# Performance work log

Hardware: AMD Instinct MI355X
Metric: run time of the kernel (lower is better)

Reference implementation:

```python
import jax, jax.numpy as jnp
import numpy as np

NEG_INF = -1.0e9
LN_EPS = 1e-5
LEAK = 0.2


def setup_inputs() -> dict:
    key = jax.random.key(0)
    ks = jax.random.split(key, 8)
    B, C, T, N, H = 8, 64, 24, 512, 2
    hd = C // H
    x = jax.random.normal(ks[0], (B, C, T, N), dtype=jnp.float32)
    gso = jax.random.randint(ks[1], (N, N), 0, 2, dtype=jnp.int32)
    # torch nn.Linear weights are (out, in); xavier-ish scale
    s = (2.0 / (C + C)) ** 0.5
    Wq = jax.random.normal(ks[2], (C, C), dtype=jnp.float32) * s
    Wk = jax.random.normal(ks[3], (C, C), dtype=jnp.float32) * s
    Wv = jax.random.normal(ks[4], (C, C), dtype=jnp.float32) * s
    sa = (2.0 / (H + hd)) ** 0.5
    a_src = jax.random.normal(ks[5], (H, hd), dtype=jnp.float32) * sa
    a_dst = jax.random.normal(ks[6], (H, hd), dtype=jnp.float32) * sa
    ln_gamma = jnp.ones((C,), dtype=jnp.float32)
    ln_beta = jnp.zeros((C,), dtype=jnp.float32)
    return {"x": x, "gso": gso, "Wq": Wq, "Wk": Wk, "Wv": Wv,
            "a_src": a_src, "a_dst": a_dst, "ln_gamma": ln_gamma, "ln_beta": ln_beta}


def _spatial_gat(x, gso, Wq, Wk, Wv, a_src, a_dst, ln_gamma, ln_beta):
    B, C, T, N = x.shape
    H, hd = a_src.shape
    # (B, C, T, N) -> (B*T, N, C)
    xr = jnp.transpose(x, (0, 2, 3, 1)).reshape(B * T, N, C)
    # torch Linear: y = x @ W.T
    Q = jnp.einsum('bnc,dc->bnd', xr, Wq).reshape(B * T, N, H, hd)
    K = jnp.einsum('bnc,dc->bnd', xr, Wk).reshape(B * T, N, H, hd)
    V = jnp.einsum('bnc,dc->bnd', xr, Wv).reshape(B * T, N, H, hd)
    # additive GAT scores, all heads at once
    s_src = jnp.einsum('bnhd,hd->bnh', Q, a_src)  # (BT, N, H)
    s_dst = jnp.einsum('bnhd,hd->bnh', K, a_dst)  # (BT, N, H)
    scores = jax.nn.leaky_relu(s_src[:, :, None, :] + s_dst[:, None, :, :], LEAK)  # (BT, Ni, Nj, H)
    mask = jnp.where(gso == 0, jnp.float32(NEG_INF), jnp.float32(0.0))  # (N, N)
    scores = scores + mask[None, :, :, None]
    attn = jax.nn.softmax(scores, axis=2)  # softmax over destination j
    out = jnp.einsum('bijh,bjhd->bihd', attn, V)  # (BT, N, H, hd)
    out = out.reshape(B * T, N, C)
    # LayerNorm over channel dim
    mu = jnp.mean(out, axis=-1, keepdims=True)
    var = jnp.var(out, axis=-1, keepdims=True)
    out = (out - mu) * jax.lax.rsqrt(var + LN_EPS) * ln_gamma + ln_beta
    # back to (B, C, T, N)
    return jnp.transpose(out.reshape(B, T, N, C), (0, 3, 1, 2))


def reference(x, gso, Wq, Wk, Wv, a_src, a_dst, ln_gamma, ln_beta):
    return _spatial_gat(x, gso, Wq, Wk, Wv, a_src, a_dst, ln_gamma, ln_beta)
```

## Files before the change

### kernel.cpp

```cpp
#include <hip/hip_runtime.h>

#define CDIM 64
#define TDIM 24
#define NDIM 512
#define NBT  192

typedef float    float4v __attribute__((ext_vector_type(4)));
typedef _Float16 half8v  __attribute__((ext_vector_type(8)));
typedef _Float16 half4v  __attribute__((ext_vector_type(4)));
typedef _Float16 half2v  __attribute__((ext_vector_type(2)));


__device__ __forceinline__ float exp2_fast(float x) {
#if __has_builtin(__builtin_amdgcn_exp2f)
  return __builtin_amdgcn_exp2f(x);
#else
  return __expf(x * 0.69314718f);
#endif
}

struct SmemK1 {
  union {
    _Float16 xt[128][72];
    _Float16 vtb[64][136];
  } big;
  _Float16 wv[64][72];
  _Float16 wext[16][72];
};

__launch_bounds__(256, 4)
__global__ void k1_v(const float* __restrict__ x,  const float* __restrict__ Wv,
                     const float* __restrict__ Wq, const float* __restrict__ Wk,
                     const float* __restrict__ a_src, const float* __restrict__ a_dst,
                     const int* __restrict__ gso,
                     _Float16* __restrict__ VT_g,
                     float* __restrict__ s_src_g, float* __restrict__ s_dst_g,
                     unsigned char* __restrict__ maskb) {
  const int t  = threadIdx.x;
  const int bx = blockIdx.x;

  if (bx >= 768) {
    int g = (bx - 768) * 256 + t;
    const int4* gp = (const int4*)gso + (size_t)g * 4;
    unsigned w[4];
#pragma unroll
    for (int k = 0; k < 4; ++k) {
      int4 v = gp[k];
      w[k] = (v.x ? 0x000000FFu : 0u) | (v.y ? 0x0000FF00u : 0u) |
             (v.z ? 0x00FF0000u : 0u) | (v.w ? 0xFF000000u : 0u);
    }
    uint4 o; o.x = w[0]; o.y = w[1]; o.z = w[2]; o.w = w[3];
    ((uint4*)maskb)[g] = o;
    return;
  }

  __shared__ SmemK1 sm;
  const int qn = bx & 3;
  const int bt = bx >> 2;
  const int b  = bt / TDIM, tt = bt % TDIM;
  const int n0 = qn * 128;

#pragma unroll
  for (int it = 0; it < 4; ++it) {
    int idx = it * 256 + t;
    float4 vv = ((const float4*)Wv)[idx];
    int d = idx >> 4, k4 = (idx & 15) * 4;
    half4v h4; h4[0] = (_Float16)vv.x; h4[1] = (_Float16)vv.y;
    h4[2] = (_Float16)vv.z; h4[3] = (_Float16)vv.w;
    *(half4v*)&sm.wv[d][k4] = h4;
  }
  for (int z = t; z < 12 * 72; z += 256) ((_Float16*)sm.wext[4])[z] = (_Float16)0.f;
  if (t < 64) {
    int c = t;
    float s0 = 0.f, s1 = 0.f, d0 = 0.f, d1 = 0.f;
#pragma unroll
    for (int d = 0; d < 32; ++d) {
      s0 += a_src[d]      * Wq[d * 64 + c];
      s1 += a_src[32 + d] * Wq[(32 + d) * 64 + c];
      d0 += a_dst[d]      * Wk[d * 64 + c];
      d1 += a_dst[32 + d] * Wk[(32 + d) * 64 + c];
    }
    const float l2e = 1.44269504f;
    sm.wext[0][c] = (_Float16)(s0 * l2e); sm.wext[1][c] = (_Float16)(s1 * l2e);
    sm.wext[2][c] = (_Float16)(d0 * l2e); sm.wext[3][c] = (_Float16)(d1 * l2e);
  }
  for (int it = 0; it < 16; ++it) {
    int idx = it * 256 + t;
    int cp = idx >> 7, n = idx & 127;
    int c0 = cp * 2;
    const float* base = x + ((size_t)(b * CDIM + c0) * TDIM + tt) * NDIM + n0 + n;
    half2v p; p[0] = (_Float16)base[0]; p[1] = (_Float16)base[(size_t)TDIM * NDIM];
    *(half2v*)&sm.big.xt[n][c0] = p;
  }
  __syncthreads();

  const int lane = t & 63, w = t >> 6;
  const int m = lane & 15, quad = lane >> 4;
  const int mbase = w * 32;

  float4v acc[2][5];
#pragma unroll
  for (int mt = 0; mt < 2; ++mt)
#pragma unroll
    for (int nt = 0; nt < 5; ++nt)
#pragma unroll
      for (int r = 0; r < 4; ++r) acc[mt][nt][r] = 0.f;

#pragma unroll
  for (int ks = 0; ks < 2; ++ks) {
    half8v af[2], bf[5];
#pragma unroll
    for (int mt = 0; mt < 2; ++mt)
      af[mt] = *(const half8v*)&sm.big.xt[mbase + mt * 16 + m][ks * 32 + quad * 8];
#pragma unroll
    for (int nt = 0; nt < 4; ++nt)
      bf[nt] = *(const half8v*)&sm.wv[nt * 16 + m][ks * 32 + quad * 8];
    bf[4] = *(const half8v*)&sm.wext[m][ks * 32 + quad * 8];
#pragma unroll
    for (int mt = 0; mt < 2; ++mt)
#pragma unroll
      for (int nt = 0; nt < 5; ++nt)
        acc[mt][nt] = __builtin_amdgcn_mfma_f32_16x16x32_f16(af[mt], bf[nt], acc[mt][nt], 0, 0, 0);
  }

  if (m < 4) {
    float* basep = (m < 2 ? s_src_g : s_dst_g) + (size_t)(bt * 2 + (m & 1)) * NDIM;
#pragma unroll
    for (int mt = 0; mt < 2; ++mt)
#pragma unroll
      for (int r = 0; r < 4; ++r)
        basep[n0 + mbase + mt * 16 + quad * 4 + r] = acc[mt][4][r];
  }
  __syncthreads();

#pragma unroll
  for (int mt = 0; mt < 2; ++mt)
#pragma unroll
    for (int nt = 0; nt < 4; ++nt)
#pragma unroll
      for (int r = 0; r < 4; r += 2) {
        int nl = mbase + mt * 16 + quad * 4 + r;
        int c  = nt * 16 + m;
        half2v p = __builtin_bit_cast(half2v,
            __builtin_amdgcn_cvt_pkrtz(acc[mt][nt][r], acc[mt][nt][r + 1]));
        *(half2v*)&sm.big.vtb[c][nl] = p;
      }
  __syncthreads();

  const uint4* vq = (const uint4*)sm.big.vtb;
#pragma unroll
  for (int it = 0; it < 4; ++it) {
    int idx = it * 256 + t;
    int c = idx >> 4, q4 = idx & 15;
    ((uint4*)VT_g)[(size_t)(bt * 64 + c) * 64 + qn * 16 + q4] = vq[c * 17 + q4];
  }
}

struct SmemK2 {
  union {
    struct { _Float16 vt[64][128]; } s;
    struct { float otile[128][66]; float rsum[2][128]; float rsq[2][128];
             float mu[128]; float rs[128]; } e;
  } u;
  _Float16 sF16[2][512];
  _Float16 sP16[2][512];
};

__launch_bounds__(256, 3)
__global__ void k2_attn(const _Float16* __restrict__ VT_g,
                        const float* __restrict__ s_src_g, const float* __restrict__ s_dst_g,
                        const unsigned char* __restrict__ maskb,
                        const float* __restrict__ gamma, const float* __restrict__ beta,
                        float* __restrict__ out) {
  __shared__ SmemK2 sm;
  const int t     = threadIdx.x;
  const int id    = blockIdx.x;
  const int itile = (id >> 3) & 3;
  const int bt    = ((id >> 5) << 3) | (id & 7);
  const int i0    = itile * 128;
  const int b     = bt / TDIM, tt = bt % TDIM;
  const int lane  = t & 63, w = t >> 6;
  const int h = w >> 1, ihalf = w & 1;
  const int m = lane & 15, quad = lane >> 4;
  const int rbase = ihalf * 64;

  for (int it = 0; it < 4; ++it) {
    int idx = it * 256 + t;
    float d = s_dst_g[(size_t)bt * 2 * NDIM + idx];
    ((_Float16*)sm.sF16)[idx] = (_Float16)exp2_fast(d);
    ((_Float16*)sm.sP16)[idx] = (_Float16)exp2_fast(0.2f * d);
  }
  half2v e2[4], q2[4];
#pragma unroll
  for (int mt = 0; mt < 4; ++mt) {
    float sv = s_src_g[(size_t)(bt * 2 + h) * NDIM + i0 + rbase + mt * 16 + m];
    _Float16 ev = (_Float16)exp2_fast(sv - 6.f);
    _Float16 qv = (_Float16)exp2_fast(0.2f * sv - 6.f);
    e2[mt][0] = ev; e2[mt][1] = ev;
    q2[mt][0] = qv; q2[mt][1] = qv;
  }

  float4v acc[4][2], accs[4];
#pragma unroll
  for (int mt = 0; mt < 4; ++mt)
#pragma unroll
    for (int r = 0; r < 4; ++r) { acc[mt][0][r] = 0.f; acc[mt][1][r] = 0.f; accs[mt][r] = 0.f; }
  const half8v bones = {(_Float16)1.f, (_Float16)1.f, (_Float16)1.f, (_Float16)1.f,
                        (_Float16)1.f, (_Float16)1.f, (_Float16)1.f, (_Float16)1.f};

  const uint4* vsrc = (const uint4*)VT_g;
  uint4 pv0, pv1, pv2, pv3;
  const int vc  = t >> 4;
  const int vch = t & 15;
  const int vswz = (vch * 8) ^ ((vc & 7) * 8);

  const unsigned char* mrow = maskb + (size_t)(i0 + rbase + m) * NDIM + quad * 8;
  uint2 mkA[4][4], mkB[4][4];

#define PREFETCH_V(js_)                                                        \
  { pv0 = vsrc[(size_t)(bt * 64 + vc     ) * 64 + (js_) * 16 + vch];           \
    pv1 = vsrc[(size_t)(bt * 64 + vc + 16) * 64 + (js_) * 16 + vch];           \
    pv2 = vsrc[(size_t)(bt * 64 + vc + 32) * 64 + (js_) * 16 + vch];           \
    pv3 = vsrc[(size_t)(bt * 64 + vc + 48) * 64 + (js_) * 16 + vch]; }

#define PREFETCH_M(mk_, js_)                                                   \
  { _Pragma("unroll")                                                          \
    for (int mt = 0; mt < 4; ++mt) {                                           \
      const unsigned char* mbp = mrow + (size_t)(mt * 16) * NDIM + (js_) * 128;\
      _Pragma("unroll")                                                        \
      for (int ksl = 0; ksl < 4; ++ksl)                                        \
        mk_[mt][ksl] = *(const uint2*)(mbp + ksl * 32);                        \
    } }

#define SLICE(mk_, js_, ksl_)                                                  \
  {                                                                            \
    const int jq = (ksl_) * 32 + quad * 8;                                     \
    half8v F8 = *(const half8v*)&sm.sF16[h][(js_) * 128 + jq];                 \
    half8v P8 = *(const half8v*)&sm.sP16[h][(js_) * 128 + jq];                 \
    const int vbase = (h * 32 + m) * 128 + (jq ^ ((m & 7) * 8));               \
    half8v b0 = *(const half8v*)&sm.u.s.vt[0][vbase];                          \
    half8v b1 = *(const half8v*)&sm.u.s.vt[0][vbase + 16 * 128];               \
    uint4 fu = __builtin_bit_cast(uint4, F8);                                  \
    uint4 pu = __builtin_bit_cast(uint4, P8);                                  \
    half2v f2a = __builtin_bit_cast(half2v, fu.x), f2b = __builtin_bit_cast(half2v, fu.y); \
    half2v f2c = __builtin_bit_cast(half2v, fu.z), f2d = __builtin_bit_cast(half2v, fu.w); \
    half2v p2a = __builtin_bit_cast(half2v, pu.x), p2b = __builtin_bit_cast(half2v, pu.y); \
    half2v p2c = __builtin_bit_cast(half2v, pu.z), p2d = __builtin_bit_cast(half2v, pu.w); \
    _Pragma("unroll")                                                          \
    for (int mt = 0; mt < 4; ++mt) {                                           \
      unsigned mw0 = mk_[mt][ksl_].x, mw1 = mk_[mt][ksl_].y;                   \
      uint4 eu;                                                                \
      eu.x = __builtin_bit_cast(unsigned,                                      \
               __builtin_elementwise_max(e2[mt] * f2a, q2[mt] * p2a)) &        \
             __builtin_amdgcn_perm(0u, mw0, 0x01010000u);                      \
      eu.y = __builtin_bit_cast(unsigned,                                      \
               __builtin_elementwise_max(e2[mt] * f2b, q2[mt] * p2b)) &        \
             __builtin_amdgcn_perm(0u, mw0, 0x03030202u);                      \
      eu.z = __builtin_bit_cast(unsigned,                                      \
               __builtin_elementwise_max(e2[mt] * f2c, q2[mt] * p2c)) &        \
             __builtin_amdgcn_perm(0u, mw1, 0x01010000u);                      \
      eu.w = __builtin_bit_cast(unsigned,                                      \
               __builtin_elementwise_max(e2[mt] * f2d, q2[mt] * p2d)) &        \
             __builtin_amdgcn_perm(0u, mw1, 0x03030202u);                      \
      half8v af = __builtin_bit_cast(half8v, eu);                              \
      acc[mt][0] = __builtin_amdgcn_mfma_f32_16x16x32_f16(af, b0,    acc[mt][0], 0, 0, 0); \
      acc[mt][1] = __builtin_amdgcn_mfma_f32_16x16x32_f16(af, b1,    acc[mt][1], 0, 0, 0); \
      accs[mt]   = __builtin_amdgcn_mfma_f32_16x16x32_f16(af, bones, accs[mt],   0, 0, 0); \
    }                                                                          \
  }

  PREFETCH_V(0);
  PREFETCH_M(mkA, 0);

#define QUARTER(mkX_, mkY_, js_)                                               \
  {                                                                            \
    __syncthreads();                          \
    *(uint4*)&sm.u.s.vt[vc     ][vswz] = pv0;                                  \
    *(uint4*)&sm.u.s.vt[vc + 16][vswz] = pv1;                                  \
    *(uint4*)&sm.u.s.vt[vc + 32][vswz] = pv2;                                  \
    *(uint4*)&sm.u.s.vt[vc + 48][vswz] = pv3;                                  \
    __syncthreads();                                                           \
    if ((js_) < 3) PREFETCH_V((js_) + 1);                                      \
    SLICE(mkX_, js_, 0);                                                       \
    SLICE(mkX_, js_, 1);                                                       \
    if ((js_) < 3) PREFETCH_M(mkY_, (js_) + 1);                                \
    SLICE(mkX_, js_, 2);                                                       \
    SLICE(mkX_, js_, 3);                                                       \
  }

  QUARTER(mkA, mkB, 0);
  QUARTER(mkB, mkA, 1);
  QUARTER(mkA, mkB, 2);
  QUARTER(mkB, mkA, 3);
#undef QUARTER
#undef SLICE
#undef PREFETCH_M
#undef PREFETCH_V

  __syncthreads();
#pragma unroll
  for (int mt = 0; mt < 4; ++mt)
#pragma unroll
    for (int r = 0; r < 4; ++r) {
      float sc = __builtin_amdgcn_rcpf(accs[mt][r]);
      int i_loc = rbase + mt * 16 + quad * 4 + r;
#pragma unroll
      for (int nt = 0; nt < 2; ++nt)
        sm.u.e.otile[i_loc][h * 32 + nt * 16 + m] = acc[mt][nt][r] * sc;
    }
  __syncthreads();

  {
    int i = t & 127, cg = t >> 7;
    float s1 = 0.f, s2 = 0.f;
#pragma unroll
    for (int cc = 0; cc < 32; ++cc) {
      float v = sm.u.e.otile[i][cg * 32 + cc];
      s1 += v; s2 += v * v;
    }
    sm.u.e.rsum[cg][i] = s1;
    sm.u.e.rsq[cg][i]  = s2;
  }
  __syncthreads();
  if (t < 128) {
    int i = t;
    float s1 = sm.u.e.rsum[0][i] + sm.u.e.rsum[1][i];
    float s2 = sm.u.e.rsq[0][i]  + sm.u.e.rsq[1][i];
    float mu  = s1 * (1.f / 64.f);
    float var = s2 * (1.f / 64.f) - mu * mu;
    sm.u.e.mu[i] = mu;
    sm.u.e.rs[i] = rsqrtf(var + 1e-5f);
  }
  __syncthreads();
  {
    int i = t & 127, cg = t >> 7;
    float mu = sm.u.e.mu[i], rs = sm.u.e.rs[i];
    int n = i0 + i;
#pragma unroll
    for (int cc = 0; cc < 32; ++cc) {
      int c = cg * 32 + cc;
      float v = (sm.u.e.otile[i][c] - mu) * rs * gamma[c] + beta[c];
      out[((size_t)(b * CDIM + c) * TDIM + tt) * NDIM + n] = v;
    }
  }
}

extern "C" void kernel_launch(void* const* d_in, const int* in_sizes, int n_in,
                              void* d_out, int out_size, void* d_ws, size_t ws_size,
                              hipStream_t stream) {
  const float* x     = (const float*)d_in[0];
  const int*   gso   = (const int*)d_in[1];
  const float* Wq    = (const float*)d_in[2];
  const float* Wk    = (const float*)d_in[3];
  const float* Wv    = (const float*)d_in[4];
  const float* a_src = (const float*)d_in[5];
  const float* a_dst = (const float*)d_in[6];
  const float* gamma = (const float*)d_in[7];
  const float* beta  = (const float*)d_in[8];
  float* out = (float*)d_out;

  char* ws = (char*)d_ws;
  _Float16* VT_g  = (_Float16*)ws;
  float*    s_src = (float*)(ws + 12582912);
  float*    s_dst = (float*)(ws + 13369344);
  unsigned char* maskb = (unsigned char*)(ws + 14155776);

  k1_v<<<832, 256, 0, stream>>>(x, Wv, Wq, Wk, a_src, a_dst, gso,
                                VT_g, s_src, s_dst, maskb);
  k2_attn<<<768, 256, 0, stream>>>(VT_g, s_src, s_dst, maskb, gamma, beta, out);
}
```

Before: 126.6 us.

## Store V in MFMA-fragment order and drop mask double-buffering

The first kernel now writes the transposed V to global memory already arranged in the per-lane MFMA B-operand fragment order. The attention kernel can then copy it into shared memory linearly and read each fragment with a contiguous lane-indexed load, without swizzle address arithmetic or bank-conflict concerns. The mask prefetch across quarters (mkA/mkB double buffering) is removed, so each quarter loads its mask bytes just before use. This lowers register pressure but exposes mask load latency.

Result: faster. 122.5 us (-3.2%).

```diff
diff --git a/kernel.cpp b/kernel.cpp
--- a/kernel.cpp
+++ b/kernel.cpp
@@ -147,18 +147,24 @@
       }
   __syncthreads();
 
-  const uint4* vq = (const uint4*)sm.big.vtb;
+  const _Float16* vtbf = (const _Float16*)sm.big.vtb;
 #pragma unroll
   for (int it = 0; it < 4; ++it) {
-    int idx = it * 256 + t;
-    int c = idx >> 4, q4 = idx & 15;
-    ((uint4*)VT_g)[(size_t)(bt * 64 + c) * 64 + qn * 16 + q4] = vq[c * 17 + q4];
+    int f    = it * 256 + t;
+    int fh   = f >> 9;
+    int fksl = (f >> 7) & 3;
+    int fb   = (f >> 6) & 1;
+    int fl   = f & 63;
+    int c  = fh * 32 + fb * 16 + (fl & 15);
+    int jq = fksl * 32 + (fl >> 4) * 8;
+    uint4 v = *(const uint4*)(vtbf + c * 136 + jq);
+    ((uint4*)VT_g)[((size_t)bt * 4 + qn) * 1024 + f] = v;
   }
 }
 
 struct SmemK2 {
   union {
-    struct { _Float16 vt[64][128]; } s;
+    _Float16 vt[8192];
     struct { float otile[128][66]; float rsum[2][128]; float rsq[2][128];
              float mu[128]; float rs[128]; } e;
   } u;
@@ -210,36 +216,22 @@
 
   const uint4* vsrc = (const uint4*)VT_g;
   uint4 pv0, pv1, pv2, pv3;
-  const int vc  = t >> 4;
-  const int vch = t & 15;
-  const int vswz = (vch * 8) ^ ((vc & 7) * 8);
 
   const unsigned char* mrow = maskb + (size_t)(i0 + rbase + m) * NDIM + quad * 8;
-  uint2 mkA[4][4], mkB[4][4];
 
 #define PREFETCH_V(js_)                                                        \
-  { pv0 = vsrc[(size_t)(bt * 64 + vc     ) * 64 + (js_) * 16 + vch];           \
-    pv1 = vsrc[(size_t)(bt * 64 + vc + 16) * 64 + (js_) * 16 + vch];           \
-    pv2 = vsrc[(size_t)(bt * 64 + vc + 32) * 64 + (js_) * 16 + vch];           \
-    pv3 = vsrc[(size_t)(bt * 64 + vc + 48) * 64 + (js_) * 16 + vch]; }
-
-#define PREFETCH_M(mk_, js_)                                                   \
-  { _Pragma("unroll")                                                          \
-    for (int mt = 0; mt < 4; ++mt) {                                           \
-      const unsigned char* mbp = mrow + (size_t)(mt * 16) * NDIM + (js_) * 128;\
-      _Pragma("unroll")                                                        \
-      for (int ksl = 0; ksl < 4; ++ksl)                                        \
-        mk_[mt][ksl] = *(const uint2*)(mbp + ksl * 32);                        \
-    } }
-
-#define SLICE(mk_, js_, ksl_)                                                  \
+  { size_t vb = ((size_t)bt * 4 + (js_)) * 1024 + t;                           \
+    pv0 = vsrc[vb];       pv1 = vsrc[vb + 256];                                \
+    pv2 = vsrc[vb + 512]; pv3 = vsrc[vb + 768]; }
+
+#define SLICE(js_, ksl_)                                                       \
   {                                                                            \
     const int jq = (ksl_) * 32 + quad * 8;                                     \
     half8v F8 = *(const half8v*)&sm.sF16[h][(js_) * 128 + jq];                 \
     half8v P8 = *(const half8v*)&sm.sP16[h][(js_) * 128 + jq];                 \
-    const int vbase = (h * 32 + m) * 128 + (jq ^ ((m & 7) * 8));               \
-    half8v b0 = *(const half8v*)&sm.u.s.vt[0][vbase];                          \
-    half8v b1 = *(const half8v*)&sm.u.s.vt[0][vbase + 16 * 128];               \
+    const int fs = ((h * 8 + (ksl_) * 2) * 64 + lane) * 8;                     \
+    half8v b0 = *(const half8v*)&sm.u.vt[fs];                                  \
+    half8v b1 = *(const half8v*)&sm.u.vt[fs + 512];                            \
     uint4 fu = __builtin_bit_cast(uint4, F8);                                  \
     uint4 pu = __builtin_bit_cast(uint4, P8);                                  \
     half2v f2a = __builtin_bit_cast(half2v, fu.x), f2b = __builtin_bit_cast(half2v, fu.y); \
@@ -248,7 +240,7 @@
     half2v p2c = __builtin_bit_cast(half2v, pu.z), p2d = __builtin_bit_cast(half2v, pu.w); \
     _Pragma("unroll")                                                          \
     for (int mt = 0; mt < 4; ++mt) {                                           \
-      unsigned mw0 = mk_[mt][ksl_].x, mw1 = mk_[mt][ksl_].y;                   \
+      unsigned mw0 = mk[mt][ksl_].x, mw1 = mk[mt][ksl_].y;                     \
       uint4 eu;                                                                \
       eu.x = __builtin_bit_cast(unsigned,                                      \
                __builtin_elementwise_max(e2[mt] * f2a, q2[mt] * p2a)) &        \
@@ -270,31 +262,32 @@
   }
 
   PREFETCH_V(0);
-  PREFETCH_M(mkA, 0);
-
-#define QUARTER(mkX_, mkY_, js_)                                               \
-  {                                                                            \
-    __syncthreads();                          \
-    *(uint4*)&sm.u.s.vt[vc     ][vswz] = pv0;                                  \
-    *(uint4*)&sm.u.s.vt[vc + 16][vswz] = pv1;                                  \
-    *(uint4*)&sm.u.s.vt[vc + 32][vswz] = pv2;                                  \
-    *(uint4*)&sm.u.s.vt[vc + 48][vswz] = pv3;                                  \
-    __syncthreads();                                                           \
-    if ((js_) < 3) PREFETCH_V((js_) + 1);                                      \
-    SLICE(mkX_, js_, 0);                                                       \
-    SLICE(mkX_, js_, 1);                                                       \
-    if ((js_) < 3) PREFETCH_M(mkY_, (js_) + 1);                                \
-    SLICE(mkX_, js_, 2);                                                       \
-    SLICE(mkX_, js_, 3);                                                       \
-  }
-
-  QUARTER(mkA, mkB, 0);
-  QUARTER(mkB, mkA, 1);
-  QUARTER(mkA, mkB, 2);
-  QUARTER(mkB, mkA, 3);
-#undef QUARTER
+
+#pragma unroll
+  for (int js = 0; js < 4; ++js) {
+    __syncthreads();
+    ((uint4*)sm.u.vt)[t      ] = pv0;
+    ((uint4*)sm.u.vt)[t + 256] = pv1;
+    ((uint4*)sm.u.vt)[t + 512] = pv2;
+    ((uint4*)sm.u.vt)[t + 768] = pv3;
+    __syncthreads();
+    if (js < 3) PREFETCH_V(js + 1);
+
+    uint2 mk[4][4];
+#pragma unroll
+    for (int mt = 0; mt < 4; ++mt) {
+      const unsigned char* mbp = mrow + (size_t)(mt * 16) * NDIM + js * 128;
+#pragma unroll
+      for (int ksl = 0; ksl < 4; ++ksl)
+        mk[mt][ksl] = *(const uint2*)(mbp + ksl * 32);
+    }
+
+    SLICE(js, 0);
+    SLICE(js, 1);
+    SLICE(js, 2);
+    SLICE(js, 3);
+  }
 #undef SLICE
-#undef PREFETCH_M
 #undef PREFETCH_V
 
   __syncthreads();
```
